# Kernel tuning notes

Hardware: AMD Instinct MI355X
Metric: run time of the kernel (lower is better)

The kernel has to match this reference:

```python
import jax, jax.numpy as jnp
import numpy as np

MARGIN = 0.3  # matches init default
EPS = 1e-12   # clamp before sqrt to avoid NaN grads at zero distance (diagonal)


def setup_inputs() -> dict:
    key = jax.random.key(0)
    k1, k2 = jax.random.split(key)
    embeddings = jax.random.normal(k1, (4096, 512), dtype=jnp.float32)
    labels = jax.random.randint(k2, (4096,), 0, 64)
    return {"embeddings": embeddings, "labels": labels}


def reference(embeddings, labels):
    # pairwise euclidean distances via the GEMM identity ||a-b||^2 = ||a||^2 + ||b||^2 - 2 a.b
    sq = jnp.sum(embeddings * embeddings, axis=1)                      # [B]
    d2 = sq[:, None] + sq[None, :] - 2.0 * (embeddings @ embeddings.T)  # [B,B]
    dist = jnp.sqrt(jnp.maximum(d2, EPS))                               # [B,B]

    eq = labels[:, None] == labels[None, :]                             # [B,B]
    eye = jnp.eye(labels.shape[0], dtype=bool)
    pos_mask = eq & ~eye
    neg_mask = ~eq

    # batch-hard mining: per-row hardest positive (max) / hardest negative (min)
    hp = jnp.max(jnp.where(pos_mask, dist, -jnp.inf), axis=1)          # [B]
    hn = jnp.min(jnp.where(neg_mask, dist, jnp.inf), axis=1)           # [B]

    valid = jnp.any(pos_mask, axis=1) & jnp.any(neg_mask, axis=1)      # [B]
    hp = jnp.where(valid, hp, 0.0)  # neutralize +/-inf on skipped rows
    hn = jnp.where(valid, hn, 0.0)

    per_row = jax.nn.relu(hp - hn + MARGIN)
    per_row = jnp.where(valid, per_row, 0.0)
    cnt = jnp.sum(valid.astype(jnp.float32))
    return jnp.where(cnt > 0, jnp.sum(per_row) / jnp.maximum(cnt, 1.0), 0.0)
```

## Files before the change

### kernel.cpp

```cpp
#include <hip/hip_runtime.h>
#include <math.h>

typedef unsigned short ushort_t;
typedef unsigned int uint_t;
typedef __attribute__((ext_vector_type(8))) short short8;
typedef __attribute__((ext_vector_type(4))) float f32x4;

#define B 4096
#define D 512
#define MARGIN 0.3f
#define EPSD 1e-12f
#define NSEG 64

__device__ inline ushort_t f2bf_rn(float x) {
    uint_t u = __float_as_uint(x);
    uint_t r = (u + 0x7fffu + ((u >> 16) & 1u)) >> 16;
    return (ushort_t)r;
}
__device__ inline void gload_lds16(const void* g, void* l) {
    __builtin_amdgcn_global_load_lds(
        (const __attribute__((address_space(1))) void*)g,
        (__attribute__((address_space(3))) void*)l, 16, 0, 0);
}

__global__ __launch_bounds__(256) void prep_kernel(const float* __restrict__ E,
                                                   float* __restrict__ sq,
                                                   ushort_t* __restrict__ Ehi,
                                                   float* __restrict__ sumcnt,
                                                   int* __restrict__ ticket) {
    int gid  = blockIdx.x * 256 + threadIdx.x;
    int w    = gid >> 6;
    int lane = gid & 63;
    const float4* row = (const float4*)(E + (size_t)w * D);
    float4 a = row[lane];
    float4 b = row[lane + 64];

    float s = a.x * a.x + a.y * a.y + a.z * a.z + a.w * a.w
            + b.x * b.x + b.y * b.y + b.z * b.z + b.w * b.w;
#pragma unroll
    for (int o = 32; o; o >>= 1) s += __shfl_down(s, o);
    if (lane == 0) sq[w] = s;

    float va[8] = {a.x, a.y, a.z, a.w, b.x, b.y, b.z, b.w};
    ushort_t hi[8];
#pragma unroll
    for (int i = 0; i < 8; ++i) hi[i] = f2bf_rn(va[i]);
    ushort4* ph = (ushort4*)(Ehi + (size_t)w * D);
    ph[lane]      = make_ushort4(hi[0], hi[1], hi[2], hi[3]);
    ph[lane + 64] = make_ushort4(hi[4], hi[5], hi[6], hi[7]);

    if (gid == 0) { sumcnt[0] = 0.f; sumcnt[1] = 0.f; ticket[0] = 0; }
}

__global__ __launch_bounds__(256) void mine_mfma(const ushort_t* __restrict__ Ehi,
                                                 const int* __restrict__ labels,
                                                 const float* __restrict__ sq,
                                                 float* __restrict__ hp_part,
                                                 float* __restrict__ hn_part) {
    __shared__ short8 a8[512];
    __shared__ short8 b8[512];
    __shared__ float  sqr_s[128], sqc_s[128];
    __shared__ int    labr_s[128], labc_s[128];
    char* aB = (char*)a8;
    char* bB = (char*)b8;

    const int tid = threadIdx.x;
    const int w   = tid >> 6;
    const int l   = tid & 63;
    const int rt  = blockIdx.x & 31;
    const int ct  = blockIdx.x >> 5;
    const int r0  = rt * 128;
    const int c0  = ct * 128;
    const int wm  = w >> 1;
    const int wn  = w & 1;

    if (tid < 128) {
        sqr_s[tid]  = sq[r0 + tid];
        labr_s[tid] = labels[r0 + tid];
    } else {
        int t = tid - 128;
        sqc_s[t]  = sq[c0 + t];
        labc_s[t] = labels[c0 + t];
    }

    f32x4 acc[4][4] = {};

    const int srow  = (l >> 2);
    const int pslot = (l & 3);

    for (int t = 0; t < 16; ++t) {
        const int kk = t * 32;
        if (t) __syncthreads();
#pragma unroll
        for (int i = 0; i < 2; ++i) {
            int rowL  = w * 32 + i * 16 + srow;
            int chunk = pslot ^ ((rowL >> 1) & 3);
            gload_lds16(Ehi + (size_t)(r0 + rowL) * D + kk + chunk * 8,
                        aB + (w * 32 + i * 16) * 64);
            gload_lds16(Ehi + (size_t)(c0 + rowL) * D + kk + chunk * 8,
                        bB + (w * 32 + i * 16) * 64);
        }
        __syncthreads();

        short8 af[4], bf[4];
#pragma unroll
        for (int f = 0; f < 4; ++f) {
            int rrA = wm * 64 + f * 16 + (l & 15);
            int sA  = (l >> 4) ^ ((rrA >> 1) & 3);
            af[f] = *(const short8*)(aB + rrA * 64 + sA * 16);
            int rrB = wn * 64 + f * 16 + (l & 15);
            int sB  = (l >> 4) ^ ((rrB >> 1) & 3);
            bf[f] = *(const short8*)(bB + rrB * 64 + sB * 16);
        }
#pragma unroll
        for (int fm = 0; fm < 4; ++fm)
#pragma unroll
            for (int fn = 0; fn < 4; ++fn)
                acc[fm][fn] = __builtin_amdgcn_mfma_f32_16x16x32_bf16(
                    af[fm], bf[fn], acc[fm][fn], 0, 0, 0);
    }

#pragma unroll
    for (int fm = 0; fm < 4; ++fm) {
        const int rbase = wm * 64 + fm * 16 + ((l >> 4) << 2);
        float hp[4], hn[4], sqr[4];
        int   labr[4];
#pragma unroll
        for (int r = 0; r < 4; ++r) {
            sqr[r]  = sqr_s[rbase + r];
            labr[r] = labr_s[rbase + r];
            hp[r] = -INFINITY;
            hn[r] =  INFINITY;
        }
#pragma unroll
        for (int fn = 0; fn < 4; ++fn) {
            const int cl   = wn * 64 + fn * 16 + (l & 15);
            const float sqc = sqc_s[cl];
            const int  labc = labc_s[cl];
            const int  gcol = c0 + cl;
#pragma unroll
            for (int r = 0; r < 4; ++r) {
                float d2   = sqr[r] + sqc - 2.f * acc[fm][fn][r];
                float dist = sqrtf(fmaxf(d2, EPSD));
                bool same  = (labr[r] == labc);
                bool diag  = ((r0 + rbase + r) == gcol);
                if (same && !diag) hp[r] = fmaxf(hp[r], dist);
                if (!same)         hn[r] = fminf(hn[r], dist);
            }
        }
#pragma unroll
        for (int r = 0; r < 4; ++r) {
#pragma unroll
            for (int m = 1; m < 16; m <<= 1) {
                hp[r] = fmaxf(hp[r], __shfl_xor(hp[r], m));
                hn[r] = fminf(hn[r], __shfl_xor(hn[r], m));
            }
        }
        if ((l & 15) == 0) {
            const int p = ct * 2 + wn;
#pragma unroll
            for (int r = 0; r < 4; ++r) {
                hp_part[(size_t)p * B + r0 + rbase + r] = hp[r];
                hn_part[(size_t)p * B + r0 + rbase + r] = hn[r];
            }
        }
    }
}

__global__ __launch_bounds__(256) void finalize_kernel(const float* __restrict__ hp_part,
                                                       const float* __restrict__ hn_part,
                                                       float* __restrict__ sumcnt,
                                                       int* __restrict__ ticket,
                                                       float* __restrict__ out) {
    const int r = blockIdx.x * 256 + threadIdx.x;
    float hp = -INFINITY, hn = INFINITY;
#pragma unroll 8
    for (int s = 0; s < NSEG; ++s) {
        hp = fmaxf(hp, hp_part[(size_t)s * B + r]);
        hn = fminf(hn, hn_part[(size_t)s * B + r]);
    }
    bool valid = (hp > -INFINITY) && (hn < INFINITY);
    float loss = valid ? fmaxf(hp - hn + MARGIN, 0.f) : 0.f;
    float cnt  = valid ? 1.f : 0.f;
#pragma unroll
    for (int o = 32; o; o >>= 1) {
        loss += __shfl_down(loss, o);
        cnt  += __shfl_down(cnt, o);
    }
    __shared__ float ls[4], cs[4];
    int lane = threadIdx.x & 63, wv = threadIdx.x >> 6;
    if (lane == 0) { ls[wv] = loss; cs[wv] = cnt; }
    __syncthreads();
    if (threadIdx.x == 0) {
        atomicAdd(&sumcnt[0], ls[0] + ls[1] + ls[2] + ls[3]);
        atomicAdd(&sumcnt[1], cs[0] + cs[1] + cs[2] + cs[3]);
        __threadfence();
        int t = atomicAdd(ticket, 1);
        if (t == (int)gridDim.x - 1) {
            float S = atomicAdd(&sumcnt[0], 0.f);
            float C = atomicAdd(&sumcnt[1], 0.f);
            out[0] = (C > 0.f) ? S / fmaxf(C, 1.f) : 0.f;
        }
    }
}

extern "C" void kernel_launch(void* const* d_in, const int* in_sizes, int n_in,
                              void* d_out, int out_size, void* d_ws, size_t ws_size,
                              hipStream_t stream) {
    const float* E      = (const float*)d_in[0];
    const int*   labels = (const int*)d_in[1];
    float* out = (float*)d_out;
    float* ws  = (float*)d_ws;

    float*    sq      = ws;
    float*    hp_part = ws + B;
    float*    hn_part = ws + B + NSEG * B;
    float*    sumcnt  = ws + B + 2 * NSEG * B;
    int*      ticket  = (int*)(ws + B + 2 * NSEG * B + 8);
    ushort_t* Ehi     = (ushort_t*)(ws + B + 2 * NSEG * B + 16);

    prep_kernel<<<B / 4, 256, 0, stream>>>(E, sq, Ehi, sumcnt, ticket);
    mine_mfma<<<32 * 32, 256, 0, stream>>>(Ehi, labels, sq, hp_part, hn_part);
    finalize_kernel<<<B / 256, 256, 0, stream>>>(hp_part, hn_part, sumcnt, ticket, out);
}
```

Baseline: 103.7 us.

## Double-buffer LDS K-loop and fuse finalize via atomic row reductions

The MFMA K-loop now double-buffers its A/B tiles in LDS. The next tile's global-to-LDS loads are issued before computing the current one, with explicit vmcnt waits and raw barriers. The separate finalize kernel and the 64-segment partial buffers are removed. Per-row hardest positive and negative are instead combined with atomicMax/atomicMin on float bit patterns (valid because distances are non-negative), and the last block, chosen by ticket, computes the loss. This saves a launch and the partial-buffer traffic, at the cost of atomic contention and a serialized final block.

```diff
diff --git a/kernel.cpp b/kernel.cpp
--- a/kernel.cpp
+++ b/kernel.cpp
@@ -10,7 +10,8 @@
 #define D 512
 #define MARGIN 0.3f
 #define EPSD 1e-12f
-#define NSEG 64
+#define NT 16
+#define GRID_MINE 1024
 
 __device__ inline ushort_t f2bf_rn(float x) {
     uint_t u = __float_as_uint(x);
@@ -26,7 +27,8 @@
 __global__ __launch_bounds__(256) void prep_kernel(const float* __restrict__ E,
                                                    float* __restrict__ sq,
                                                    ushort_t* __restrict__ Ehi,
-                                                   float* __restrict__ sumcnt,
+                                                   uint_t* __restrict__ hp_bits,
+                                                   uint_t* __restrict__ hn_bits,
                                                    int* __restrict__ ticket) {
     int gid  = blockIdx.x * 256 + threadIdx.x;
     int w    = gid >> 6;
@@ -49,20 +51,23 @@
     ph[lane]      = make_ushort4(hi[0], hi[1], hi[2], hi[3]);
     ph[lane + 64] = make_ushort4(hi[4], hi[5], hi[6], hi[7]);
 
-    if (gid == 0) { sumcnt[0] = 0.f; sumcnt[1] = 0.f; ticket[0] = 0; }
+    if (gid < B) { hp_bits[gid] = 0u; hn_bits[gid] = 0x7f800000u; }
+    if (gid == 0) ticket[0] = 0;
 }
 
 __global__ __launch_bounds__(256) void mine_mfma(const ushort_t* __restrict__ Ehi,
                                                  const int* __restrict__ labels,
                                                  const float* __restrict__ sq,
-                                                 float* __restrict__ hp_part,
-                                                 float* __restrict__ hn_part) {
-    __shared__ short8 a8[512];
-    __shared__ short8 b8[512];
+                                                 uint_t* __restrict__ hp_bits,
+                                                 uint_t* __restrict__ hn_bits,
+                                                 int* __restrict__ ticket,
+                                                 float* __restrict__ out) {
+    __shared__ char aB[2][8192];
+    __shared__ char bB[2][8192];
     __shared__ float  sqr_s[128], sqc_s[128];
     __shared__ int    labr_s[128], labc_s[128];
-    char* aB = (char*)a8;
-    char* bB = (char*)b8;
+    __shared__ float  red_s[8];
+    __shared__ int    last_s;
 
     const int tid = threadIdx.x;
     const int w   = tid >> 6;
@@ -88,29 +93,47 @@
     const int srow  = (l >> 2);
     const int pslot = (l & 3);
 
-    for (int t = 0; t < 16; ++t) {
-        const int kk = t * 32;
-        if (t) __syncthreads();
-#pragma unroll
-        for (int i = 0; i < 2; ++i) {
-            int rowL  = w * 32 + i * 16 + srow;
-            int chunk = pslot ^ ((rowL >> 1) & 3);
-            gload_lds16(Ehi + (size_t)(r0 + rowL) * D + kk + chunk * 8,
-                        aB + (w * 32 + i * 16) * 64);
-            gload_lds16(Ehi + (size_t)(c0 + rowL) * D + kk + chunk * 8,
-                        bB + (w * 32 + i * 16) * 64);
-        }
-        __syncthreads();
+#pragma unroll
+    for (int i = 0; i < 2; ++i) {
+        int rowL  = w * 32 + i * 16 + srow;
+        int chunk = pslot ^ ((rowL >> 1) & 3);
+        gload_lds16(Ehi + (size_t)(r0 + rowL) * D + 0 + chunk * 8,
+                    aB[0] + (w * 32 + i * 16) * 64);
+        gload_lds16(Ehi + (size_t)(c0 + rowL) * D + 0 + chunk * 8,
+                    bB[0] + (w * 32 + i * 16) * 64);
+    }
+
+#pragma unroll
+    for (int t = 0; t < NT; ++t) {
+        const int cur = t & 1;
+        if (t + 1 < NT) {
+            const int nb = (t + 1) & 1;
+            const int kk = (t + 1) * 32;
+#pragma unroll
+            for (int i = 0; i < 2; ++i) {
+                int rowL  = w * 32 + i * 16 + srow;
+                int chunk = pslot ^ ((rowL >> 1) & 3);
+                gload_lds16(Ehi + (size_t)(r0 + rowL) * D + kk + chunk * 8,
+                            aB[nb] + (w * 32 + i * 16) * 64);
+                gload_lds16(Ehi + (size_t)(c0 + rowL) * D + kk + chunk * 8,
+                            bB[nb] + (w * 32 + i * 16) * 64);
+            }
+            asm volatile("s_waitcnt vmcnt(4)" ::: "memory");
+        } else {
+            asm volatile("s_waitcnt vmcnt(0)" ::: "memory");
+        }
+        __builtin_amdgcn_s_barrier();
+        __builtin_amdgcn_sched_barrier(0);
 
         short8 af[4], bf[4];
 #pragma unroll
         for (int f = 0; f < 4; ++f) {
             int rrA = wm * 64 + f * 16 + (l & 15);
             int sA  = (l >> 4) ^ ((rrA >> 1) & 3);
-            af[f] = *(const short8*)(aB + rrA * 64 + sA * 16);
+            af[f] = *(const short8*)(aB[cur] + rrA * 64 + sA * 16);
             int rrB = wn * 64 + f * 16 + (l & 15);
             int sB  = (l >> 4) ^ ((rrB >> 1) & 3);
-            bf[f] = *(const short8*)(bB + rrB * 64 + sB * 16);
+            bf[f] = *(const short8*)(bB[cur] + rrB * 64 + sB * 16);
         }
 #pragma unroll
         for (int fm = 0; fm < 4; ++fm)
@@ -118,6 +141,10 @@
             for (int fn = 0; fn < 4; ++fn)
                 acc[fm][fn] = __builtin_amdgcn_mfma_f32_16x16x32_bf16(
                     af[fm], bf[fn], acc[fm][fn], 0, 0, 0);
+
+        __builtin_amdgcn_sched_barrier(0);
+        __builtin_amdgcn_s_barrier();
+        __builtin_amdgcn_sched_barrier(0);
     }
 
 #pragma unroll
@@ -157,48 +184,43 @@
             }
         }
         if ((l & 15) == 0) {
-            const int p = ct * 2 + wn;
 #pragma unroll
             for (int r = 0; r < 4; ++r) {
-                hp_part[(size_t)p * B + r0 + rbase + r] = hp[r];
-                hn_part[(size_t)p * B + r0 + rbase + r] = hn[r];
-            }
-        }
-    }
-}
-
-__global__ __launch_bounds__(256) void finalize_kernel(const float* __restrict__ hp_part,
-                                                       const float* __restrict__ hn_part,
-                                                       float* __restrict__ sumcnt,
-                                                       int* __restrict__ ticket,
-                                                       float* __restrict__ out) {
-    const int r = blockIdx.x * 256 + threadIdx.x;
-    float hp = -INFINITY, hn = INFINITY;
-#pragma unroll 8
-    for (int s = 0; s < NSEG; ++s) {
-        hp = fmaxf(hp, hp_part[(size_t)s * B + r]);
-        hn = fminf(hn, hn_part[(size_t)s * B + r]);
-    }
-    bool valid = (hp > -INFINITY) && (hn < INFINITY);
-    float loss = valid ? fmaxf(hp - hn + MARGIN, 0.f) : 0.f;
-    float cnt  = valid ? 1.f : 0.f;
-#pragma unroll
-    for (int o = 32; o; o >>= 1) {
-        loss += __shfl_down(loss, o);
-        cnt  += __shfl_down(cnt, o);
-    }
-    __shared__ float ls[4], cs[4];
-    int lane = threadIdx.x & 63, wv = threadIdx.x >> 6;
-    if (lane == 0) { ls[wv] = loss; cs[wv] = cnt; }
+                const int row = r0 + rbase + r;
+                if (hp[r] >= 0.f)
+                    atomicMax(&hp_bits[row], __float_as_uint(hp[r]));
+                if (hn[r] < INFINITY)
+                    atomicMin(&hn_bits[row], __float_as_uint(hn[r]));
+            }
+        }
+    }
+
+    __threadfence();
     __syncthreads();
-    if (threadIdx.x == 0) {
-        atomicAdd(&sumcnt[0], ls[0] + ls[1] + ls[2] + ls[3]);
-        atomicAdd(&sumcnt[1], cs[0] + cs[1] + cs[2] + cs[3]);
-        __threadfence();
-        int t = atomicAdd(ticket, 1);
-        if (t == (int)gridDim.x - 1) {
-            float S = atomicAdd(&sumcnt[0], 0.f);
-            float C = atomicAdd(&sumcnt[1], 0.f);
+    if (tid == 0) last_s = (atomicAdd(ticket, 1) == GRID_MINE - 1);
+    __syncthreads();
+    if (last_s) {
+        float sum = 0.f, cnt = 0.f;
+#pragma unroll
+        for (int r = tid; r < B; r += 256) {
+            uint_t hpb = atomicOr(&hp_bits[r], 0u);
+            uint_t hnb = atomicOr(&hn_bits[r], 0u);
+            if (hpb != 0u && hnb != 0x7f800000u) {
+                sum += fmaxf(__uint_as_float(hpb) - __uint_as_float(hnb) + MARGIN, 0.f);
+                cnt += 1.f;
+            }
+        }
+#pragma unroll
+        for (int o = 32; o; o >>= 1) {
+            sum += __shfl_down(sum, o);
+            cnt += __shfl_down(cnt, o);
+        }
+        int lane = tid & 63, wv = tid >> 6;
+        if (lane == 0) { red_s[wv] = sum; red_s[4 + wv] = cnt; }
+        __syncthreads();
+        if (tid == 0) {
+            float S = red_s[0] + red_s[1] + red_s[2] + red_s[3];
+            float C = red_s[4] + red_s[5] + red_s[6] + red_s[7];
             out[0] = (C > 0.f) ? S / fmaxf(C, 1.f) : 0.f;
         }
     }
@@ -213,13 +235,11 @@
     float* ws  = (float*)d_ws;
 
     float*    sq      = ws;
-    float*    hp_part = ws + B;
-    float*    hn_part = ws + B + NSEG * B;
-    float*    sumcnt  = ws + B + 2 * NSEG * B;
-    int*      ticket  = (int*)(ws + B + 2 * NSEG * B + 8);
-    ushort_t* Ehi     = (ushort_t*)(ws + B + 2 * NSEG * B + 16);
-
-    prep_kernel<<<B / 4, 256, 0, stream>>>(E, sq, Ehi, sumcnt, ticket);
-    mine_mfma<<<32 * 32, 256, 0, stream>>>(Ehi, labels, sq, hp_part, hn_part);
-    finalize_kernel<<<B / 256, 256, 0, stream>>>(hp_part, hn_part, sumcnt, ticket, out);
-}
+    uint_t*   hp_bits = (uint_t*)(ws + B);
+    uint_t*   hn_bits = (uint_t*)(ws + 2 * B);
+    int*      ticket  = (int*)(ws + 3 * B);
+    ushort_t* Ehi     = (ushort_t*)(ws + 3 * B + 16);
+
+    prep_kernel<<<B / 4, 256, 0, stream>>>(E, sq, Ehi, hp_bits, hn_bits, ticket);
+    mine_mfma<<<GRID_MINE, 256, 0, stream>>>(Ehi, labels, sq, hp_bits, hn_bits, ticket, out);
+}
```

New measurement: 158.9 us. +53.3%, slower.

## Load MFMA operands directly from global memory instead of staging through LDS

Applied to the files above, without the earlier changes.

Removes the LDS staging buffers and global_load_lds copies in the GEMM mining kernel. Each wave now reads its bf16 A/B fragments straight from global memory (relying on L2/L1 cache), which drops the two barriers per K step, and the K loop is unrolled by two. The trade-off is that tiles are no longer shared across waves, so each row fragment is fetched by two waves and global traffic rises. The 16-byte per-lane reads are also less coalesced.

```diff
diff --git a/kernel.cpp b/kernel.cpp
--- a/kernel.cpp
+++ b/kernel.cpp
@@ -16,11 +16,6 @@
     uint_t u = __float_as_uint(x);
     uint_t r = (u + 0x7fffu + ((u >> 16) & 1u)) >> 16;
     return (ushort_t)r;
-}
-__device__ inline void gload_lds16(const void* g, void* l) {
-    __builtin_amdgcn_global_load_lds(
-        (const __attribute__((address_space(1))) void*)g,
-        (__attribute__((address_space(3))) void*)l, 16, 0, 0);
 }
 
 __global__ __launch_bounds__(256) void prep_kernel(const float* __restrict__ E,
@@ -57,12 +52,8 @@
                                                  const float* __restrict__ sq,
                                                  float* __restrict__ hp_part,
                                                  float* __restrict__ hn_part) {
-    __shared__ short8 a8[512];
-    __shared__ short8 b8[512];
-    __shared__ float  sqr_s[128], sqc_s[128];
-    __shared__ int    labr_s[128], labc_s[128];
-    char* aB = (char*)a8;
-    char* bB = (char*)b8;
+    __shared__ float sqr_s[128], sqc_s[128];
+    __shared__ int   labr_s[128], labc_s[128];
 
     const int tid = threadIdx.x;
     const int w   = tid >> 6;
@@ -78,40 +69,30 @@
         sqr_s[tid]  = sq[r0 + tid];
         labr_s[tid] = labels[r0 + tid];
     } else {
-        int t = tid - 128;
-        sqc_s[t]  = sq[c0 + t];
-        labc_s[t] = labels[c0 + t];
+        int q = tid - 128;
+        sqc_s[q]  = sq[c0 + q];
+        labc_s[q] = labels[c0 + q];
+    }
+    __syncthreads();
+
+    const ushort_t* aP[4];
+    const ushort_t* bP[4];
+#pragma unroll
+    for (int f = 0; f < 4; ++f) {
+        aP[f] = Ehi + (size_t)(r0 + wm * 64 + f * 16 + (l & 15)) * D + (l >> 4) * 8;
+        bP[f] = Ehi + (size_t)(c0 + wn * 64 + f * 16 + (l & 15)) * D + (l >> 4) * 8;
     }
 
     f32x4 acc[4][4] = {};
 
-    const int srow  = (l >> 2);
-    const int pslot = (l & 3);
-
+#pragma unroll 2
     for (int t = 0; t < 16; ++t) {
         const int kk = t * 32;
-        if (t) __syncthreads();
-#pragma unroll
-        for (int i = 0; i < 2; ++i) {
-            int rowL  = w * 32 + i * 16 + srow;
-            int chunk = pslot ^ ((rowL >> 1) & 3);
-            gload_lds16(Ehi + (size_t)(r0 + rowL) * D + kk + chunk * 8,
-                        aB + (w * 32 + i * 16) * 64);
-            gload_lds16(Ehi + (size_t)(c0 + rowL) * D + kk + chunk * 8,
-                        bB + (w * 32 + i * 16) * 64);
-        }
-        __syncthreads();
-
         short8 af[4], bf[4];
 #pragma unroll
-        for (int f = 0; f < 4; ++f) {
-            int rrA = wm * 64 + f * 16 + (l & 15);
-            int sA  = (l >> 4) ^ ((rrA >> 1) & 3);
-            af[f] = *(const short8*)(aB + rrA * 64 + sA * 16);
-            int rrB = wn * 64 + f * 16 + (l & 15);
-            int sB  = (l >> 4) ^ ((rrB >> 1) & 3);
-            bf[f] = *(const short8*)(bB + rrB * 64 + sB * 16);
-        }
+        for (int f = 0; f < 4; ++f) af[f] = *(const short8*)(aP[f] + kk);
+#pragma unroll
+        for (int f = 0; f < 4; ++f) bf[f] = *(const short8*)(bP[f] + kk);
 #pragma unroll
         for (int fm = 0; fm < 4; ++fm)
 #pragma unroll
```

New measurement: 133.5 us. +28.7%, slower.
